# Optimization experiments

Hardware: AMD Instinct MI355X
Metric: run time of the kernel (lower is better)

Reference implementation:

```python
import jax, jax.numpy as jnp
import numpy as np

T, D_IN, D_HID, D_OUT = 8192, 1024, 2048, 1024
C = 8


def setup_inputs() -> dict:
    key = jax.random.key(0)
    ks = jax.random.split(key, 10)
    min_a = 0.99 ** (1.0 / C)
    max_a = 0.999 ** (1.0 / C)
    s_in = 1.0 / np.sqrt(D_IN)
    s_hid = 1.0 / np.sqrt(D_HID)
    return {
        "inputs": jax.random.normal(ks[0], (T, D_IN), dtype=jnp.float32),
        "pre_a": jax.random.uniform(ks[1], (D_HID,), dtype=jnp.float32) * (max_a - min_a) + min_a,
        "Wr": jax.random.normal(ks[2], (D_HID, D_IN), dtype=jnp.float32) * s_in,
        "br": jax.random.normal(ks[3], (D_HID,), dtype=jnp.float32) * s_in,
        "Wi": jax.random.normal(ks[4], (D_HID, D_IN), dtype=jnp.float32) * s_in,
        "bi": jax.random.normal(ks[5], (D_HID,), dtype=jnp.float32) * s_in,
        "Wx": jax.random.normal(ks[6], (D_HID, D_IN), dtype=jnp.float32) * s_in,
        "bx": jax.random.normal(ks[7], (D_HID,), dtype=jnp.float32) * s_in,
        "Wo": jax.random.normal(ks[8], (D_OUT, D_HID), dtype=jnp.float32) * s_hid,
        "bo": jax.random.normal(ks[9], (D_OUT,), dtype=jnp.float32) * s_hid,
    }


def reference(inputs, pre_a, Wr, br, Wi, bi, Wx, bx, Wo, bo):
    # inputs: [T, d_in]; all gates/states: [T, d_hidden]
    r_t = jax.nn.sigmoid(inputs @ Wr.T + br)            # recurrence gate
    i_t = jax.nn.sigmoid(inputs @ Wi.T + bi)            # input gate
    a_t = jnp.exp(-C * jax.nn.softplus(pre_a) * r_t)    # decay in (0,1)
    x = inputs @ Wx.T + bx
    gated_x = jnp.sqrt(1.0 - jnp.square(a_t)) * (i_t * x)

    def combine(q_i, q_j):
        A_i, b_i_ = q_i
        A_j, b_j_ = q_j
        return (A_j * A_i, A_j * b_i_ + b_j_)

    _, hidden_states = jax.lax.associative_scan(combine, (a_t, gated_x), axis=0)
    return hidden_states @ Wo.T + bo                    # [T, d_out]
```

## Files before the change

### kernel.cpp

```cpp
#include <hip/hip_runtime.h>
#include <cstdint>
#include <cstddef>

#define TT 8192
#define DIN 1024
#define DHID 2048
#define DOUT 1024
#define NCHUNK 128
#define CLEN 64

typedef __bf16 bf16x8 __attribute__((ext_vector_type(8)));
typedef float f32x4 __attribute__((ext_vector_type(4)));
using u32_as1 = __attribute__((address_space(1))) const unsigned int;
using u32_as3 = __attribute__((address_space(3))) unsigned int;

__device__ __forceinline__ unsigned short bf16r(float x) {
  unsigned int u = __float_as_uint(x);
  u += 0x7fffu + ((u >> 16) & 1u);
  return (unsigned short)(u >> 16);
}

__device__ __forceinline__ float bf16tof(unsigned short u) {
  return __uint_as_float(((unsigned int)u) << 16);
}

__global__ void cast_f32_bf16(const float* __restrict__ in, unsigned short* __restrict__ out, int n4) {
  int i = blockIdx.x * 256 + threadIdx.x;
  if (i >= n4) return;
  const float4 v = reinterpret_cast<const float4*>(in)[i];
  ushort4 o;
  o.x = bf16r(v.x);
  o.y = bf16r(v.y);
  o.z = bf16r(v.z);
  o.w = bf16r(v.w);
  reinterpret_cast<ushort4*>(out)[i] = o;
}

__global__ void dec_kernel(const float* __restrict__ pre_a, float* __restrict__ dec) {
  const int d = blockIdx.x * 256 + threadIdx.x;
  if (d < DHID) dec[d] = -8.0f * log1pf(expf(pre_a[d]));
}

__global__ __launch_bounds__(256) void gemm_gates(
    const unsigned short* __restrict__ X, const unsigned short* __restrict__ Wr,
    const unsigned short* __restrict__ Wi, const unsigned short* __restrict__ Wx,
    const float* __restrict__ br, const float* __restrict__ bi, const float* __restrict__ bx,
    const float* __restrict__ dec, float* __restrict__ a_out, unsigned short* __restrict__ gx_out) {
  __shared__ __align__(16) unsigned short lds[(128 + 3 * 64) * 32];
  const int n0 = blockIdx.x * 64;
  const int t0 = blockIdx.y * 128;
  const int tid = threadIdx.x;
  const int wave = tid >> 6, lane = tid & 63;
  const int wr = wave >> 1, wc = wave & 1;
  const int row16 = lane & 15, kq = lane >> 4;

  f32x4 acc[3][4][2] = {};

  for (int k0 = 0; k0 < DIN; k0 += 32) {
#pragma unroll
    for (int s = 0; s < 5; ++s) {
      const int seg = wave * 5 + s;
      const int lb = lane * 16;
      if (seg < 8) {
        const int off = seg * 1024 + lb;
        const int row = off >> 6, ke = (off & 63) >> 1;
        __builtin_amdgcn_global_load_lds((u32_as1*)(X + (size_t)(t0 + row) * DIN + k0 + ke),
                                         (u32_as3*)(lds + seg * 512), 16, 0, 0);
      } else {
        const int m = (seg - 8) >> 2, sub = (seg - 8) & 3;
        const unsigned short* Bm = (m == 0) ? Wr : ((m == 1) ? Wi : Wx);
        const int off = sub * 1024 + lb;
        const int row = off >> 6, ke = (off & 63) >> 1;
        __builtin_amdgcn_global_load_lds((u32_as1*)(Bm + (size_t)(n0 + row) * DIN + k0 + ke),
                                         (u32_as3*)(lds + (128 + m * 64) * 32 + sub * 512), 16, 0, 0);
      }
    }
    __syncthreads();

    const unsigned short* Ab = lds + (wr * 64 + row16) * 32 + kq * 8;
    bf16x8 af[4];
#pragma unroll
    for (int mf = 0; mf < 4; ++mf) af[mf] = *reinterpret_cast<const bf16x8*>(Ab + mf * 16 * 32);
#pragma unroll
    for (int z = 0; z < 3; ++z) {
      const unsigned short* Bb = lds + (128 + z * 64 + wc * 32 + row16) * 32 + kq * 8;
      const bf16x8 b0 = *reinterpret_cast<const bf16x8*>(Bb);
      const bf16x8 b1 = *reinterpret_cast<const bf16x8*>(Bb + 16 * 32);
#pragma unroll
      for (int mf = 0; mf < 4; ++mf) {
        acc[z][mf][0] = __builtin_amdgcn_mfma_f32_16x16x32_bf16(af[mf], b0, acc[z][mf][0], 0, 0, 0);
        acc[z][mf][1] = __builtin_amdgcn_mfma_f32_16x16x32_bf16(af[mf], b1, acc[z][mf][1], 0, 0, 0);
      }
    }
    __syncthreads();
  }

#pragma unroll
  for (int nf = 0; nf < 2; ++nf) {
    const int n = n0 + wc * 32 + nf * 16 + row16;
    const float brv = br[n], biv = bi[n], bxv = bx[n], dcv = dec[n];
#pragma unroll
    for (int mf = 0; mf < 4; ++mf) {
#pragma unroll
      for (int r = 0; r < 4; ++r) {
        const int t = t0 + wr * 64 + mf * 16 + kq * 4 + r;
        const float rp = acc[0][mf][nf][r] + brv;
        const float ip = acc[1][mf][nf][r] + biv;
        const float xv = acc[2][mf][nf][r] + bxv;
        const float rs = __builtin_amdgcn_rcpf(1.0f + __expf(-rp));
        const float av = __expf(dcv * rs);
        const float is = __builtin_amdgcn_rcpf(1.0f + __expf(-ip));
        const float gv = sqrtf(fmaxf(0.0f, 1.0f - av * av)) * (is * xv);
        a_out[(size_t)t * DHID + n] = av;
        gx_out[(size_t)t * DHID + n] = bf16r(gv);
      }
    }
  }
}

template <int KDIM, int NDIM>
__global__ __launch_bounds__(256) void gemm_bt(const unsigned short* __restrict__ A,
                                               const unsigned short* __restrict__ B,
                                               const float* __restrict__ bias,
                                               float* __restrict__ out) {
  __shared__ __align__(16) unsigned short Alds[128 * 32];
  __shared__ __align__(16) unsigned short Blds[128 * 32];
  const int n0 = blockIdx.x * 128;
  const int t0 = blockIdx.y * 128;
  const int tid = threadIdx.x;
  const int wave = tid >> 6, lane = tid & 63;
  const int wr = wave >> 1, wc = wave & 1;
  const int row16 = lane & 15, kq = lane >> 4;

  f32x4 acc[4][4] = {};

  for (int k0 = 0; k0 < KDIM; k0 += 32) {
#pragma unroll
    for (int s = 0; s < 2; ++s) {
      const int seg = wave * 2 + s;
      const int off = seg * 1024 + lane * 16;
      const int row = off >> 6;
      const int ke = (off & 63) >> 1;
      __builtin_amdgcn_global_load_lds((u32_as1*)(A + (size_t)(t0 + row) * KDIM + k0 + ke),
                                       (u32_as3*)(Alds + seg * 512), 16, 0, 0);
      __builtin_amdgcn_global_load_lds((u32_as1*)(B + (size_t)(n0 + row) * KDIM + k0 + ke),
                                       (u32_as3*)(Blds + seg * 512), 16, 0, 0);
    }
    __syncthreads();

    const unsigned short* Ab = Alds + (wr * 64 + row16) * 32 + kq * 8;
    const unsigned short* Bb = Blds + (wc * 64 + row16) * 32 + kq * 8;
    bf16x8 af[4], bfr[4];
#pragma unroll
    for (int mf = 0; mf < 4; ++mf) af[mf] = *reinterpret_cast<const bf16x8*>(Ab + mf * 16 * 32);
#pragma unroll
    for (int nf = 0; nf < 4; ++nf) bfr[nf] = *reinterpret_cast<const bf16x8*>(Bb + nf * 16 * 32);
#pragma unroll
    for (int mf = 0; mf < 4; ++mf)
#pragma unroll
      for (int nf = 0; nf < 4; ++nf)
        acc[mf][nf] = __builtin_amdgcn_mfma_f32_16x16x32_bf16(af[mf], bfr[nf], acc[mf][nf], 0, 0, 0);
    __syncthreads();
  }

#pragma unroll
  for (int mf = 0; mf < 4; ++mf) {
#pragma unroll
    for (int nf = 0; nf < 4; ++nf) {
      const int n = n0 + wc * 64 + nf * 16 + row16;
      const float bs = bias[n];
#pragma unroll
      for (int r = 0; r < 4; ++r) {
        const int t = t0 + wr * 64 + mf * 16 + kq * 4 + r;
        out[(size_t)t * NDIM + n] = acc[mf][nf][r] + bs;
      }
    }
  }
}

__global__ void scan_pass1(const float* __restrict__ a, const unsigned short* __restrict__ gx,
                           float* __restrict__ aggA, float* __restrict__ aggB) {
  const int d = blockIdx.y * 256 + threadIdx.x;
  const int c = blockIdx.x;
  const size_t base = (size_t)c * CLEN * DHID + d;
  float h = 0.0f, p = 1.0f;
#pragma unroll 4
  for (int t = 0; t < CLEN; ++t) {
    const float av = a[base + (size_t)t * DHID];
    const float bv = bf16tof(gx[base + (size_t)t * DHID]);
    h = fmaf(av, h, bv);
    p *= av;
  }
  aggA[c * DHID + d] = p;
  aggB[c * DHID + d] = h;
}

__global__ void scan_pass2(const float* __restrict__ aggA, const float* __restrict__ aggB,
                           float* __restrict__ pref) {
  const int d = blockIdx.x * 256 + threadIdx.x;
  float p = 0.0f;
  for (int c = 0; c < NCHUNK; ++c) {
    p = fmaf(aggA[c * DHID + d], p, aggB[c * DHID + d]);
    pref[c * DHID + d] = p;
  }
}

__global__ void scan_pass3(const float* __restrict__ a, const unsigned short* __restrict__ gx,
                           const float* __restrict__ pref, unsigned short* __restrict__ hbf) {
  const int d = blockIdx.y * 256 + threadIdx.x;
  const int c = blockIdx.x;
  float h = (c == 0) ? 0.0f : pref[(c - 1) * DHID + d];
  const size_t base = (size_t)c * CLEN * DHID + d;
#pragma unroll 4
  for (int t = 0; t < CLEN; ++t) {
    const float av = a[base + (size_t)t * DHID];
    const float bv = bf16tof(gx[base + (size_t)t * DHID]);
    h = fmaf(av, h, bv);
    hbf[base + (size_t)t * DHID] = bf16r(h);
  }
}

extern "C" void kernel_launch(void* const* d_in, const int* in_sizes, int n_in,
                              void* d_out, int out_size, void* d_ws, size_t ws_size,
                              hipStream_t stream) {
  const float* inputs = (const float*)d_in[0];
  const float* pre_a = (const float*)d_in[1];
  const float* Wr = (const float*)d_in[2];
  const float* br = (const float*)d_in[3];
  const float* Wi = (const float*)d_in[4];
  const float* bi = (const float*)d_in[5];
  const float* Wx = (const float*)d_in[6];
  const float* bx = (const float*)d_in[7];
  const float* Wo = (const float*)d_in[8];
  const float* bo = (const float*)d_in[9];
  float* out = (float*)d_out;

  char* ws = (char*)d_ws;
  size_t off = 0;
  auto alloc = [&](size_t bytes) {
    char* p = ws + off;
    off += (bytes + 255) & ~(size_t)255;
    return p;
  };
  unsigned short* Xbf = (unsigned short*)alloc((size_t)TT * DIN * 2);
  unsigned short* Wrbf = (unsigned short*)alloc((size_t)DHID * DIN * 2);
  unsigned short* Wibf = (unsigned short*)alloc((size_t)DHID * DIN * 2);
  unsigned short* Wxbf = (unsigned short*)alloc((size_t)DHID * DIN * 2);
  unsigned short* Wobf = (unsigned short*)alloc((size_t)DOUT * DHID * 2);
  float* a_buf = (float*)alloc((size_t)TT * DHID * 4);
  unsigned short* gx_buf = (unsigned short*)alloc((size_t)TT * DHID * 2);
  unsigned short* hbf = (unsigned short*)alloc((size_t)TT * DHID * 2);
  float* dec = (float*)alloc(DHID * 4);
  float* aggA = (float*)alloc((size_t)NCHUNK * DHID * 4);
  float* aggB = (float*)alloc((size_t)NCHUNK * DHID * 4);
  float* pref = (float*)alloc((size_t)NCHUNK * DHID * 4);
  if (off > ws_size) return;

  cast_f32_bf16<<<TT * DIN / 4 / 256, 256, 0, stream>>>(inputs, Xbf, TT * DIN / 4);
  cast_f32_bf16<<<DHID * DIN / 4 / 256, 256, 0, stream>>>(Wr, Wrbf, DHID * DIN / 4);
  cast_f32_bf16<<<DHID * DIN / 4 / 256, 256, 0, stream>>>(Wi, Wibf, DHID * DIN / 4);
  cast_f32_bf16<<<DHID * DIN / 4 / 256, 256, 0, stream>>>(Wx, Wxbf, DHID * DIN / 4);
  cast_f32_bf16<<<DOUT * DHID / 4 / 256, 256, 0, stream>>>(Wo, Wobf, DOUT * DHID / 4);
  dec_kernel<<<DHID / 256, 256, 0, stream>>>(pre_a, dec);

  gemm_gates<<<dim3(DHID / 64, TT / 128), 256, 0, stream>>>(Xbf, Wrbf, Wibf, Wxbf, br, bi, bx, dec,
                                                            a_buf, gx_buf);

  scan_pass1<<<dim3(NCHUNK, DHID / 256), 256, 0, stream>>>(a_buf, gx_buf, aggA, aggB);
  scan_pass2<<<DHID / 256, 256, 0, stream>>>(aggA, aggB, pref);
  scan_pass3<<<dim3(NCHUNK, DHID / 256), 256, 0, stream>>>(a_buf, gx_buf, pref, hbf);

  gemm_bt<DHID, DOUT><<<dim3(DOUT / 128, TT / 128), 256, 0, stream>>>(hbf, Wobf, bo, out);
}
```

Before: 254.7 us.

## Triple-buffer gate GEMM LDS with async prefetch and XOR swizzle

Restructures the gate GEMM main loop to use three LDS buffers, issuing global-to-LDS loads two k-tiles ahead and waiting with explicit vmcnt counts instead of two full syncthreads per iteration. Adds an XOR swizzle on the k column to reduce LDS bank conflicts on fragment reads, and raises wave priority around the MFMA block. The larger LDS footprint and the launch bound of 2 may limit occupancy and cap registers.

```diff
diff --git a/kernel.cpp b/kernel.cpp
--- a/kernel.cpp
+++ b/kernel.cpp
@@ -8,6 +8,8 @@
 #define DOUT 1024
 #define NCHUNK 128
 #define CLEN 64
+#define NT 32
+#define BUFE 10240
 
 typedef __bf16 bf16x8 __attribute__((ext_vector_type(8)));
 typedef float f32x4 __attribute__((ext_vector_type(4)));
@@ -41,58 +43,84 @@
   if (d < DHID) dec[d] = -8.0f * log1pf(expf(pre_a[d]));
 }
 
-__global__ __launch_bounds__(256) void gemm_gates(
+__global__ __launch_bounds__(256, 2) void gemm_gates(
     const unsigned short* __restrict__ X, const unsigned short* __restrict__ Wr,
     const unsigned short* __restrict__ Wi, const unsigned short* __restrict__ Wx,
     const float* __restrict__ br, const float* __restrict__ bi, const float* __restrict__ bx,
     const float* __restrict__ dec, float* __restrict__ a_out, unsigned short* __restrict__ gx_out) {
-  __shared__ __align__(16) unsigned short lds[(128 + 3 * 64) * 32];
+  __shared__ __align__(16) unsigned short lds[3 * BUFE];
   const int n0 = blockIdx.x * 64;
   const int t0 = blockIdx.y * 128;
   const int tid = threadIdx.x;
   const int wave = tid >> 6, lane = tid & 63;
   const int wr = wave >> 1, wc = wave & 1;
   const int row16 = lane & 15, kq = lane >> 4;
+  const int swz = (row16 & 3) << 3;
+  const int scol = ((lane & 3) ^ ((lane >> 2) & 3)) << 3;
+  const int lrow = lane >> 2;
 
   f32x4 acc[3][4][2] = {};
 
-  for (int k0 = 0; k0 < DIN; k0 += 32) {
+  auto stage = [&](int kt, int sbase) {
+    const int kbase = kt * 32 + scol;
 #pragma unroll
     for (int s = 0; s < 5; ++s) {
       const int seg = wave * 5 + s;
-      const int lb = lane * 16;
       if (seg < 8) {
-        const int off = seg * 1024 + lb;
-        const int row = off >> 6, ke = (off & 63) >> 1;
-        __builtin_amdgcn_global_load_lds((u32_as1*)(X + (size_t)(t0 + row) * DIN + k0 + ke),
-                                         (u32_as3*)(lds + seg * 512), 16, 0, 0);
+        const int row = seg * 16 + lrow;
+        __builtin_amdgcn_global_load_lds((u32_as1*)(X + (size_t)(t0 + row) * DIN + kbase),
+                                         (u32_as3*)(lds + sbase + seg * 512), 16, 0, 0);
       } else {
-        const int m = (seg - 8) >> 2, sub = (seg - 8) & 3;
+        const int m = (seg - 8) >> 2, sl = (seg - 8) & 3;
         const unsigned short* Bm = (m == 0) ? Wr : ((m == 1) ? Wi : Wx);
-        const int off = sub * 1024 + lb;
-        const int row = off >> 6, ke = (off & 63) >> 1;
-        __builtin_amdgcn_global_load_lds((u32_as1*)(Bm + (size_t)(n0 + row) * DIN + k0 + ke),
-                                         (u32_as3*)(lds + (128 + m * 64) * 32 + sub * 512), 16, 0, 0);
+        const int row = sl * 16 + lrow;
+        __builtin_amdgcn_global_load_lds((u32_as1*)(Bm + (size_t)(n0 + row) * DIN + kbase),
+                                         (u32_as3*)(lds + sbase + seg * 512), 16, 0, 0);
       }
     }
-    __syncthreads();
-
-    const unsigned short* Ab = lds + (wr * 64 + row16) * 32 + kq * 8;
-    bf16x8 af[4];
-#pragma unroll
-    for (int mf = 0; mf < 4; ++mf) af[mf] = *reinterpret_cast<const bf16x8*>(Ab + mf * 16 * 32);
-#pragma unroll
-    for (int z = 0; z < 3; ++z) {
-      const unsigned short* Bb = lds + (128 + z * 64 + wc * 32 + row16) * 32 + kq * 8;
-      const bf16x8 b0 = *reinterpret_cast<const bf16x8*>(Bb);
-      const bf16x8 b1 = *reinterpret_cast<const bf16x8*>(Bb + 16 * 32);
-#pragma unroll
-      for (int mf = 0; mf < 4; ++mf) {
-        acc[z][mf][0] = __builtin_amdgcn_mfma_f32_16x16x32_bf16(af[mf], b0, acc[z][mf][0], 0, 0, 0);
-        acc[z][mf][1] = __builtin_amdgcn_mfma_f32_16x16x32_bf16(af[mf], b1, acc[z][mf][1], 0, 0, 0);
-      }
-    }
-    __syncthreads();
+  };
+
+  stage(0, 0);
+  stage(1, BUFE);
+  asm volatile("s_waitcnt vmcnt(5)" ::: "memory");
+  __builtin_amdgcn_s_barrier();
+  __builtin_amdgcn_sched_barrier(0);
+
+  int cb = 0, sb = 2 * BUFE;
+  for (int t = 0; t < NT; ++t) {
+    if (t < NT - 2) stage(t + 2, sb);
+
+    bf16x8 af[4], bfr[3][2];
+#pragma unroll
+    for (int mf = 0; mf < 4; ++mf)
+      af[mf] = *reinterpret_cast<const bf16x8*>(lds + cb + (wr * 64 + mf * 16 + row16) * 32 +
+                                                ((kq * 8) ^ swz));
+#pragma unroll
+    for (int z = 0; z < 3; ++z)
+#pragma unroll
+      for (int nf = 0; nf < 2; ++nf)
+        bfr[z][nf] = *reinterpret_cast<const bf16x8*>(lds + cb + 4096 + z * 2048 +
+                                                      (wc * 32 + nf * 16 + row16) * 32 +
+                                                      ((kq * 8) ^ swz));
+    __builtin_amdgcn_s_setprio(1);
+#pragma unroll
+    for (int z = 0; z < 3; ++z)
+#pragma unroll
+      for (int mf = 0; mf < 4; ++mf)
+#pragma unroll
+        for (int nf = 0; nf < 2; ++nf)
+          acc[z][mf][nf] = __builtin_amdgcn_mfma_f32_16x16x32_bf16(af[mf], bfr[z][nf], acc[z][mf][nf], 0, 0, 0);
+    __builtin_amdgcn_s_setprio(0);
+
+    if (t < NT - 2) {
+      asm volatile("s_waitcnt vmcnt(5)" ::: "memory");
+    } else {
+      asm volatile("s_waitcnt vmcnt(0)" ::: "memory");
+    }
+    __builtin_amdgcn_s_barrier();
+    __builtin_amdgcn_sched_barrier(0);
+    cb = (cb == 2 * BUFE) ? 0 : cb + BUFE;
+    sb = (sb == 2 * BUFE) ? 0 : sb + BUFE;
   }
 
 #pragma unroll
```

Measured after the change: 729.1 us. +186.2%, slower.

## Double-buffer LDS tiles in gate and output GEMMs to overlap loads with MFMA

Applied to the files above, without the earlier changes.

Both the fused gate GEMM and the output GEMM now keep two shared-memory tile buffers. Each iteration issues the direct-to-LDS global loads for the next K tile before running the MFMAs on the current one, and a single barrier per iteration replaces the previous load-then-wait-then-compute sequence. The goal is to hide global-memory latency behind matrix math. In exchange it doubles LDS use (about 40 KB for the gate kernel), which may reduce how many blocks fit on each CU.

```diff
diff --git a/kernel.cpp b/kernel.cpp
--- a/kernel.cpp
+++ b/kernel.cpp
@@ -8,6 +8,8 @@
 #define DOUT 1024
 #define NCHUNK 128
 #define CLEN 64
+#define NT 32
+#define BUFE 10240
 
 typedef __bf16 bf16x8 __attribute__((ext_vector_type(8)));
 typedef float f32x4 __attribute__((ext_vector_type(4)));
@@ -46,7 +48,7 @@
     const unsigned short* __restrict__ Wi, const unsigned short* __restrict__ Wx,
     const float* __restrict__ br, const float* __restrict__ bi, const float* __restrict__ bx,
     const float* __restrict__ dec, float* __restrict__ a_out, unsigned short* __restrict__ gx_out) {
-  __shared__ __align__(16) unsigned short lds[(128 + 3 * 64) * 32];
+  __shared__ __align__(16) unsigned short lds[2 * BUFE];
   const int n0 = blockIdx.x * 64;
   const int t0 = blockIdx.y * 128;
   const int tid = threadIdx.x;
@@ -56,7 +58,8 @@
 
   f32x4 acc[3][4][2] = {};
 
-  for (int k0 = 0; k0 < DIN; k0 += 32) {
+  auto stage = [&](int kt, int sbase) {
+    const int k0 = kt * 32;
 #pragma unroll
     for (int s = 0; s < 5; ++s) {
       const int seg = wave * 5 + s;
@@ -65,25 +68,32 @@
         const int off = seg * 1024 + lb;
         const int row = off >> 6, ke = (off & 63) >> 1;
         __builtin_amdgcn_global_load_lds((u32_as1*)(X + (size_t)(t0 + row) * DIN + k0 + ke),
-                                         (u32_as3*)(lds + seg * 512), 16, 0, 0);
+                                         (u32_as3*)(lds + sbase + seg * 512), 16, 0, 0);
       } else {
         const int m = (seg - 8) >> 2, sub = (seg - 8) & 3;
         const unsigned short* Bm = (m == 0) ? Wr : ((m == 1) ? Wi : Wx);
         const int off = sub * 1024 + lb;
         const int row = off >> 6, ke = (off & 63) >> 1;
         __builtin_amdgcn_global_load_lds((u32_as1*)(Bm + (size_t)(n0 + row) * DIN + k0 + ke),
-                                         (u32_as3*)(lds + (128 + m * 64) * 32 + sub * 512), 16, 0, 0);
-      }
-    }
-    __syncthreads();
-
-    const unsigned short* Ab = lds + (wr * 64 + row16) * 32 + kq * 8;
+                                         (u32_as3*)(lds + sbase + (128 + m * 64) * 32 + sub * 512), 16, 0, 0);
+      }
+    }
+  };
+
+  stage(0, 0);
+  __syncthreads();
+
+  for (int t = 0; t < NT; ++t) {
+    const int cb = (t & 1) * BUFE;
+    if (t + 1 < NT) stage(t + 1, ((t + 1) & 1) * BUFE);
+
+    const unsigned short* Ab = lds + cb + (wr * 64 + row16) * 32 + kq * 8;
     bf16x8 af[4];
 #pragma unroll
     for (int mf = 0; mf < 4; ++mf) af[mf] = *reinterpret_cast<const bf16x8*>(Ab + mf * 16 * 32);
 #pragma unroll
     for (int z = 0; z < 3; ++z) {
-      const unsigned short* Bb = lds + (128 + z * 64 + wc * 32 + row16) * 32 + kq * 8;
+      const unsigned short* Bb = lds + cb + (128 + z * 64 + wc * 32 + row16) * 32 + kq * 8;
       const bf16x8 b0 = *reinterpret_cast<const bf16x8*>(Bb);
       const bf16x8 b1 = *reinterpret_cast<const bf16x8*>(Bb + 16 * 32);
 #pragma unroll
@@ -123,18 +133,20 @@
                                                const unsigned short* __restrict__ B,
                                                const float* __restrict__ bias,
                                                float* __restrict__ out) {
-  __shared__ __align__(16) unsigned short Alds[128 * 32];
-  __shared__ __align__(16) unsigned short Blds[128 * 32];
+  __shared__ __align__(16) unsigned short Alds[2][128 * 32];
+  __shared__ __align__(16) unsigned short Blds[2][128 * 32];
   const int n0 = blockIdx.x * 128;
   const int t0 = blockIdx.y * 128;
   const int tid = threadIdx.x;
   const int wave = tid >> 6, lane = tid & 63;
   const int wr = wave >> 1, wc = wave & 1;
   const int row16 = lane & 15, kq = lane >> 4;
+  constexpr int KT = KDIM / 32;
 
   f32x4 acc[4][4] = {};
 
-  for (int k0 = 0; k0 < KDIM; k0 += 32) {
+  auto stage = [&](int kt, int buf) {
+    const int k0 = kt * 32;
 #pragma unroll
     for (int s = 0; s < 2; ++s) {
       const int seg = wave * 2 + s;
@@ -142,14 +154,21 @@
       const int row = off >> 6;
       const int ke = (off & 63) >> 1;
       __builtin_amdgcn_global_load_lds((u32_as1*)(A + (size_t)(t0 + row) * KDIM + k0 + ke),
-                                       (u32_as3*)(Alds + seg * 512), 16, 0, 0);
+                                       (u32_as3*)(Alds[buf] + seg * 512), 16, 0, 0);
       __builtin_amdgcn_global_load_lds((u32_as1*)(B + (size_t)(n0 + row) * KDIM + k0 + ke),
-                                       (u32_as3*)(Blds + seg * 512), 16, 0, 0);
-    }
-    __syncthreads();
-
-    const unsigned short* Ab = Alds + (wr * 64 + row16) * 32 + kq * 8;
-    const unsigned short* Bb = Blds + (wc * 64 + row16) * 32 + kq * 8;
+                                       (u32_as3*)(Blds[buf] + seg * 512), 16, 0, 0);
+    }
+  };
+
+  stage(0, 0);
+  __syncthreads();
+
+  for (int t = 0; t < KT; ++t) {
+    const int cb = t & 1;
+    if (t + 1 < KT) stage(t + 1, (t + 1) & 1);
+
+    const unsigned short* Ab = Alds[cb] + (wr * 64 + row16) * 32 + kq * 8;
+    const unsigned short* Bb = Blds[cb] + (wc * 64 + row16) * 32 + kq * 8;
     bf16x8 af[4], bfr[4];
 #pragma unroll
     for (int mf = 0; mf < 4; ++mf) af[mf] = *reinterpret_cast<const bf16x8*>(Ab + mf * 16 * 32);
```

Measured after the change: 454.9 us. 78.6% more time.

## Pack decay and gated input into one bf16 pair word; vectorize scan passes

Applied to the files above, without the earlier changes.

The gate GEMM now stores 1-a and the gated input as two bf16 values packed into one 32-bit word, replacing the separate fp32 decay buffer and bf16 input buffer. Scan traffic falls from 6 to 4 bytes per element in each of the two chunk passes. Each scan thread now handles two hidden channels with 64-bit loads and packed stores, and the four weight casts are merged into one launch. Storing 1-a in bf16 keeps some precision for a near 1, but the decay is still coarser than fp32, which adds scan error. Pass 2 uses half as many threads.

```diff
diff --git a/kernel.cpp b/kernel.cpp
--- a/kernel.cpp
+++ b/kernel.cpp
@@ -20,8 +20,8 @@
   return (unsigned short)(u >> 16);
 }
 
-__device__ __forceinline__ float bf16tof(unsigned short u) {
-  return __uint_as_float(((unsigned int)u) << 16);
+__device__ __forceinline__ float bf16tof(unsigned int u) {
+  return __uint_as_float(u << 16);
 }
 
 __global__ void cast_f32_bf16(const float* __restrict__ in, unsigned short* __restrict__ out, int n4) {
@@ -36,6 +36,23 @@
   reinterpret_cast<ushort4*>(out)[i] = o;
 }
 
+__global__ void cast_w4(const float* __restrict__ s0, const float* __restrict__ s1,
+                        const float* __restrict__ s2, const float* __restrict__ s3,
+                        unsigned short* __restrict__ d0, unsigned short* __restrict__ d1,
+                        unsigned short* __restrict__ d2, unsigned short* __restrict__ d3) {
+  const int y = blockIdx.y;
+  const float* s = (y == 0) ? s0 : ((y == 1) ? s1 : ((y == 2) ? s2 : s3));
+  unsigned short* d = (y == 0) ? d0 : ((y == 1) ? d1 : ((y == 2) ? d2 : d3));
+  const int i = blockIdx.x * 256 + threadIdx.x;
+  const float4 v = reinterpret_cast<const float4*>(s)[i];
+  ushort4 o;
+  o.x = bf16r(v.x);
+  o.y = bf16r(v.y);
+  o.z = bf16r(v.z);
+  o.w = bf16r(v.w);
+  reinterpret_cast<ushort4*>(d)[i] = o;
+}
+
 __global__ void dec_kernel(const float* __restrict__ pre_a, float* __restrict__ dec) {
   const int d = blockIdx.x * 256 + threadIdx.x;
   if (d < DHID) dec[d] = -8.0f * log1pf(expf(pre_a[d]));
@@ -45,7 +62,7 @@
     const unsigned short* __restrict__ X, const unsigned short* __restrict__ Wr,
     const unsigned short* __restrict__ Wi, const unsigned short* __restrict__ Wx,
     const float* __restrict__ br, const float* __restrict__ bi, const float* __restrict__ bx,
-    const float* __restrict__ dec, float* __restrict__ a_out, unsigned short* __restrict__ gx_out) {
+    const float* __restrict__ dec, unsigned int* __restrict__ pack_out) {
   __shared__ __align__(16) unsigned short lds[(128 + 3 * 64) * 32];
   const int n0 = blockIdx.x * 64;
   const int t0 = blockIdx.y * 128;
@@ -111,8 +128,8 @@
         const float av = __expf(dcv * rs);
         const float is = __builtin_amdgcn_rcpf(1.0f + __expf(-ip));
         const float gv = sqrtf(fmaxf(0.0f, 1.0f - av * av)) * (is * xv);
-        a_out[(size_t)t * DHID + n] = av;
-        gx_out[(size_t)t * DHID + n] = bf16r(gv);
+        const float om = 1.0f - av;
+        pack_out[(size_t)t * DHID + n] = ((unsigned int)bf16r(gv) << 16) | (unsigned int)bf16r(om);
       }
     }
   }
@@ -178,45 +195,62 @@
   }
 }
 
-__global__ void scan_pass1(const float* __restrict__ a, const unsigned short* __restrict__ gx,
+__global__ void scan_pass1(const unsigned int* __restrict__ pack,
                            float* __restrict__ aggA, float* __restrict__ aggB) {
-  const int d = blockIdx.y * 256 + threadIdx.x;
+  const int d0 = blockIdx.y * 512 + threadIdx.x * 2;
   const int c = blockIdx.x;
-  const size_t base = (size_t)c * CLEN * DHID + d;
-  float h = 0.0f, p = 1.0f;
+  const size_t base = (size_t)c * CLEN * DHID + d0;
+  float h0 = 0.0f, h1 = 0.0f, p0 = 1.0f, p1 = 1.0f;
 #pragma unroll 4
   for (int t = 0; t < CLEN; ++t) {
-    const float av = a[base + (size_t)t * DHID];
-    const float bv = bf16tof(gx[base + (size_t)t * DHID]);
-    h = fmaf(av, h, bv);
-    p *= av;
-  }
-  aggA[c * DHID + d] = p;
-  aggB[c * DHID + d] = h;
+    const uint2 v = *reinterpret_cast<const uint2*>(pack + base + (size_t)t * DHID);
+    const float a0 = 1.0f - bf16tof(v.x & 0xffffu);
+    const float a1 = 1.0f - bf16tof(v.y & 0xffffu);
+    h0 = fmaf(a0, h0, bf16tof(v.x >> 16));
+    h1 = fmaf(a1, h1, bf16tof(v.y >> 16));
+    p0 *= a0;
+    p1 *= a1;
+  }
+  *reinterpret_cast<float2*>(aggA + c * DHID + d0) = make_float2(p0, p1);
+  *reinterpret_cast<float2*>(aggB + c * DHID + d0) = make_float2(h0, h1);
 }
 
 __global__ void scan_pass2(const float* __restrict__ aggA, const float* __restrict__ aggB,
                            float* __restrict__ pref) {
-  const int d = blockIdx.x * 256 + threadIdx.x;
-  float p = 0.0f;
+  const int d0 = blockIdx.x * 512 + threadIdx.x * 2;
+  float p0 = 0.0f, p1 = 0.0f;
+#pragma unroll 8
   for (int c = 0; c < NCHUNK; ++c) {
-    p = fmaf(aggA[c * DHID + d], p, aggB[c * DHID + d]);
-    pref[c * DHID + d] = p;
-  }
-}
-
-__global__ void scan_pass3(const float* __restrict__ a, const unsigned short* __restrict__ gx,
-                           const float* __restrict__ pref, unsigned short* __restrict__ hbf) {
-  const int d = blockIdx.y * 256 + threadIdx.x;
+    const float2 A = *reinterpret_cast<const float2*>(aggA + c * DHID + d0);
+    const float2 B = *reinterpret_cast<const float2*>(aggB + c * DHID + d0);
+    p0 = fmaf(A.x, p0, B.x);
+    p1 = fmaf(A.y, p1, B.y);
+    *reinterpret_cast<float2*>(pref + c * DHID + d0) = make_float2(p0, p1);
+  }
+}
+
+__global__ void scan_pass3(const unsigned int* __restrict__ pack, const float* __restrict__ pref,
+                           unsigned int* __restrict__ hbf2 ) {
+  const int d0 = blockIdx.y * 512 + threadIdx.x * 2;
   const int c = blockIdx.x;
-  float h = (c == 0) ? 0.0f : pref[(c - 1) * DHID + d];
-  const size_t base = (size_t)c * CLEN * DHID + d;
+  float h0, h1;
+  if (c == 0) {
+    h0 = 0.0f;
+    h1 = 0.0f;
+  } else {
+    const float2 pv = *reinterpret_cast<const float2*>(pref + (c - 1) * DHID + d0);
+    h0 = pv.x;
+    h1 = pv.y;
+  }
+  const size_t base = (size_t)c * CLEN * DHID + d0;
 #pragma unroll 4
   for (int t = 0; t < CLEN; ++t) {
-    const float av = a[base + (size_t)t * DHID];
-    const float bv = bf16tof(gx[base + (size_t)t * DHID]);
-    h = fmaf(av, h, bv);
-    hbf[base + (size_t)t * DHID] = bf16r(h);
+    const uint2 v = *reinterpret_cast<const uint2*>(pack + base + (size_t)t * DHID);
+    const float a0 = 1.0f - bf16tof(v.x & 0xffffu);
+    const float a1 = 1.0f - bf16tof(v.y & 0xffffu);
+    h0 = fmaf(a0, h0, bf16tof(v.x >> 16));
+    h1 = fmaf(a1, h1, bf16tof(v.y >> 16));
+    hbf2[(base + (size_t)t * DHID) >> 1] = ((unsigned int)bf16r(h1) << 16) | (unsigned int)bf16r(h0);
   }
 }
 
@@ -247,8 +281,7 @@
   unsigned short* Wibf = (unsigned short*)alloc((size_t)DHID * DIN * 2);
   unsigned short* Wxbf = (unsigned short*)alloc((size_t)DHID * DIN * 2);
   unsigned short* Wobf = (unsigned short*)alloc((size_t)DOUT * DHID * 2);
-  float* a_buf = (float*)alloc((size_t)TT * DHID * 4);
-  unsigned short* gx_buf = (unsigned short*)alloc((size_t)TT * DHID * 2);
+  unsigned int* pack = (unsigned int*)alloc((size_t)TT * DHID * 4);
   unsigned short* hbf = (unsigned short*)alloc((size_t)TT * DHID * 2);
   float* dec = (float*)alloc(DHID * 4);
   float* aggA = (float*)alloc((size_t)NCHUNK * DHID * 4);
@@ -257,18 +290,15 @@
   if (off > ws_size) return;
 
   cast_f32_bf16<<<TT * DIN / 4 / 256, 256, 0, stream>>>(inputs, Xbf, TT * DIN / 4);
-  cast_f32_bf16<<<DHID * DIN / 4 / 256, 256, 0, stream>>>(Wr, Wrbf, DHID * DIN / 4);
-  cast_f32_bf16<<<DHID * DIN / 4 / 256, 256, 0, stream>>>(Wi, Wibf, DHID * DIN / 4);
-  cast_f32_bf16<<<DHID * DIN / 4 / 256, 256, 0, stream>>>(Wx, Wxbf, DHID * DIN / 4);
-  cast_f32_bf16<<<DOUT * DHID / 4 / 256, 256, 0, stream>>>(Wo, Wobf, DOUT * DHID / 4);
+  cast_w4<<<dim3(DHID * DIN / 4 / 256, 4), 256, 0, stream>>>(Wr, Wi, Wx, Wo, Wrbf, Wibf, Wxbf, Wobf);
   dec_kernel<<<DHID / 256, 256, 0, stream>>>(pre_a, dec);
 
   gemm_gates<<<dim3(DHID / 64, TT / 128), 256, 0, stream>>>(Xbf, Wrbf, Wibf, Wxbf, br, bi, bx, dec,
-                                                            a_buf, gx_buf);
-
-  scan_pass1<<<dim3(NCHUNK, DHID / 256), 256, 0, stream>>>(a_buf, gx_buf, aggA, aggB);
-  scan_pass2<<<DHID / 256, 256, 0, stream>>>(aggA, aggB, pref);
-  scan_pass3<<<dim3(NCHUNK, DHID / 256), 256, 0, stream>>>(a_buf, gx_buf, pref, hbf);
+                                                            pack);
+
+  scan_pass1<<<dim3(NCHUNK, DHID / 512), 256, 0, stream>>>(pack, aggA, aggB);
+  scan_pass2<<<DHID / 512, 256, 0, stream>>>(aggA, aggB, pref);
+  scan_pass3<<<dim3(NCHUNK, DHID / 512), 256, 0, stream>>>(pack, pref, (unsigned int*)hbf);
 
   gemm_bt<DHID, DOUT><<<dim3(DOUT / 128, TT / 128), 256, 0, stream>>>(hbf, Wobf, bo, out);
 }
```

After: 245.9 us. -3.5%, faster.
